# Performance work log

Measured on AMD Instinct MI355X. Metric: run time of the kernel, lower is better.

Reference implementation:

```python
import jax, jax.numpy as jnp
import numpy as np

B, S, D, H, O = 256, 64, 256, 1024, 512
N_CELLS = 3


def setup_inputs() -> dict:
    key = jax.random.key(0)
    ks = jax.random.split(key, 16)

    def u(k, shape, fan):
        return (jax.random.uniform(k, shape, jnp.float32, -1.0, 1.0) / np.float32(np.sqrt(fan)))

    inp = {"inputs": jax.random.normal(ks[0], (B, S, D), jnp.float32)}
    in_dims = [D, H, H]
    i = 1
    for c in range(N_CELLS):
        inp[f"w_ih_{c}"] = u(ks[i], (3 * H, in_dims[c]), H); i += 1
        inp[f"w_hh_{c}"] = u(ks[i], (3 * H, H), H); i += 1
        inp[f"b_ih_{c}"] = u(ks[i], (3 * H,), H); i += 1
        inp[f"b_hh_{c}"] = u(ks[i], (3 * H,), H); i += 1
    inp["lin_w"] = u(ks[13], (S, H, O), H)   # per-step linear weights (same_linear=False)
    inp["lin_b"] = u(ks[14], (S, O), H)
    return inp


def _gru_cell(x, h, w_ih, w_hh, b_ih, b_hh):
    # PyTorch GRUCell gate order: r, z, n
    gi = x @ w_ih.T + b_ih          # [B, 3H]
    gh = h @ w_hh.T + b_hh          # [B, 3H]
    i_r, i_z, i_n = jnp.split(gi, 3, axis=-1)
    h_r, h_z, h_n = jnp.split(gh, 3, axis=-1)
    r = jax.nn.sigmoid(i_r + h_r)
    z = jax.nn.sigmoid(i_z + h_z)
    n = jnp.tanh(i_n + r * h_n)
    return (1.0 - z) * n + z * h


def reference(inputs, w_ih_0, w_hh_0, b_ih_0, b_hh_0,
              w_ih_1, w_hh_1, b_ih_1, b_hh_1,
              w_ih_2, w_hh_2, b_ih_2, b_hh_2,
              lin_w, lin_b):
    params = [(w_ih_0, w_hh_0, b_ih_0, b_hh_0),
              (w_ih_1, w_hh_1, b_ih_1, b_hh_1),
              (w_ih_2, w_hh_2, b_ih_2, b_hh_2)]
    batch = inputs.shape[0]
    hdim = w_hh_0.shape[1]

    def step(hs, xs):
        x_t, wL, bL = xs              # [B,D], [H,O], [O]
        new_hs = []
        cur = x_t
        for i, (wi, wh, bi, bh) in enumerate(params):
            h = _gru_cell(cur, hs[i], wi, wh, bi, bh)
            new_hs.append(h)
            cur = h
        out = cur @ wL + bL           # [B,O]
        return tuple(new_hs), out

    h0 = tuple(jnp.zeros((batch, hdim), inputs.dtype) for _ in range(N_CELLS))
    xs = (jnp.swapaxes(inputs, 0, 1), lin_w, lin_b)  # scan over seq dim
    hs, outs = jax.lax.scan(step, h0, xs)            # outs: [S,B,O]
    return (jnp.swapaxes(outs, 0, 1), hs[0], hs[1], hs[2])
```

## Files before the change

### kernel.cpp

```cpp
#include <hip/hip_runtime.h>
#include <hip/hip_bf16.h>
#include <stdint.h>

#define B_ 256
#define S_ 64
#define D_ 256
#define H_ 1024
#define O_ 512
#define G_ 3072
#define BH_ (B_ * H_)

typedef unsigned short u16;
typedef __attribute__((ext_vector_type(8))) short bf16x8;
typedef __attribute__((ext_vector_type(4))) float f32x4;

#define MFMA16(a, b, c) __builtin_amdgcn_mfma_f32_16x16x32_bf16((a), (b), (c), 0, 0, 0)

__device__ __forceinline__ u16 f2b(float f) {
    union { float f; uint32_t u; } v; v.f = f;
    uint32_t u = v.u;
    return (u16)((u + 0x7fffu + ((u >> 16) & 1u)) >> 16);
}

__device__ __forceinline__ void gl_lds16(const u16* g, u16* l) {
    __builtin_amdgcn_global_load_lds(
        (const __attribute__((address_space(1))) unsigned int*)g,
        (__attribute__((address_space(3))) unsigned int*)l, 16, 0, 0);
}
__device__ __forceinline__ unsigned long long sysld64(const u16* p) {
    return __hip_atomic_load((const unsigned long long*)p, __ATOMIC_RELAXED, __HIP_MEMORY_SCOPE_SYSTEM);
}
__device__ __forceinline__ void sysst64(u16* p, unsigned long long v) {
    __hip_atomic_store((unsigned long long*)p, v, __ATOMIC_RELAXED, __HIP_MEMORY_SCOPE_SYSTEM);
}
__device__ __forceinline__ void waitflag(int* f, int n) {
    while (__hip_atomic_load(f, __ATOMIC_RELAXED, __HIP_MEMORY_SCOPE_SYSTEM) < n)
        __builtin_amdgcn_s_sleep(8);
    asm volatile("" ::: "memory");
}
__device__ __forceinline__ void postflag(int* f) {
    __hip_atomic_fetch_add(f, 1, __ATOMIC_RELAXED, __HIP_MEMORY_SCOPE_SYSTEM);
}


__global__ void k_conv(const float* __restrict__ s, u16* __restrict__ d, int n4) {
    int i = blockIdx.x * blockDim.x + threadIdx.x;
    int st = gridDim.x * blockDim.x;
    for (; i < n4; i += st) {
        float4 v = ((const float4*)s)[i];
        ushort4 o;
        o.x = f2b(v.x); o.y = f2b(v.y); o.z = f2b(v.z); o.w = f2b(v.w);
        ((ushort4*)d)[i] = o;
    }
}

__global__ __launch_bounds__(256) void k_twl(const float* __restrict__ w, u16* __restrict__ o) {
    __shared__ float tile[32][33];
    int bid = blockIdx.x;
    int t = bid >> 9;
    int rem = bid & 511;
    int j0 = (rem >> 4) << 5;
    int o0 = (rem & 15) << 5;
    int tx = threadIdx.x & 31, ty = threadIdx.x >> 5;
    const float* base = w + (size_t)t * (H_ * O_);
#pragma unroll
    for (int i = 0; i < 4; ++i) {
        int r = ty + (i << 3);
        tile[r][tx] = base[(size_t)(j0 + r) * O_ + o0 + tx];
    }
    __syncthreads();
    u16* ob = o + (size_t)t * (O_ * H_);
#pragma unroll
    for (int i = 0; i < 4; ++i) {
        int r = ty + (i << 3);
        ob[(size_t)(o0 + r) * H_ + j0 + tx] = f2b(tile[tx][r]);
    }
}


struct GruArgs {
    const u16* Xb;
    const u16 *Wi0, *Wh0, *Wi1, *Wh1, *Wi2, *Wh2;
    const float *bi0, *bh0, *bi1, *bh1, *bi2, *bh2;
    u16 *h0, *h1, *h2a;
    const u16* WLt;
    const float* lb;
    float* out;
    int* ready;
    int* consumed;
};

__global__ __launch_bounds__(512, 1) void k_gru(GruArgs p) {
    __shared__ u16 Wb[2][3][128 * 64];
    __shared__ u16 Ab[2][32 * 64];
    __shared__ float carry[32 * 132];

    const int w = blockIdx.x;
    const int g = w & 7;
    const int slot = w >> 3;
    const int role = slot >> 3;
    const int sub = slot & 7;
    const int b0 = g * 32;

    const int tid = threadIdx.x;
    const int wid = tid >> 6, lane = tid & 63;
    const int fr = lane & 15, kc = lane >> 4;

    const int arow = tid >> 4;
    const int acol = (tid & 15) << 2;
    const int adst = arow * 64 + ((((tid & 15) >> 1) ^ (arow & 7)) << 3) + ((tid & 1) << 2);

    int sw0 = ((kc ^ (fr & 7)) << 3);
    int sw1 = (((4 + kc) ^ (fr & 7)) << 3);

    int* ready = p.ready + g * 3 * 64;
    int* consumed = p.consumed + g * 2 * 64;

    for (int i = tid; i < 32 * 132; i += 512) carry[i] = 0.f;
    __syncthreads();

    if (role < 3) {
        const u16 *Wi, *Wh; const float *bi, *bh; int K0;
        if (role == 0)      { Wi = p.Wi0; Wh = p.Wh0; bi = p.bi0; bh = p.bh0; K0 = D_; }
        else if (role == 1) { Wi = p.Wi1; Wh = p.Wh1; bi = p.bi1; bh = p.bh1; K0 = H_; }
        else                { Wi = p.Wi2; Wh = p.Wh2; bi = p.bi2; bh = p.bh2; K0 = H_; }
        const int nXc = K0 >> 6;
        const int nC = nXc + 16;
        const int j0 = sub * 128;
        const int jme = j0 + (wid << 4) + fr;
        const float b_r = bi[jme] + bh[jme];
        const float b_z = bi[H_ + jme] + bh[H_ + jme];
        const float b_i = bi[2 * H_ + jme];
        const float b_h = bh[2 * H_ + jme];

        const u16 *A0 = nullptr, *Ah = nullptr; int ld0 = H_;
        u16* hout = nullptr;

        auto LA = [&](int c) -> unsigned long long {
            const u16* s = (c < nXc) ? (A0 + (size_t)arow * ld0 + (c << 6) + acol)
                                     : (Ah + (size_t)arow * H_ + ((c - nXc) << 6) + acol);
            return sysld64(s);
        };
        auto SW = [&](int c, int nb) {
            if (c < nXc) {
                int ko = c << 6;
#pragma unroll
                for (int hh = 0; hh < 2; ++hh) {
                    int ci = (hh << 9) + tid, jr = ci >> 3, c8 = ci & 7;
                    size_t ro = (size_t)(j0 + jr) * K0 + ko + ((c8 ^ (jr & 7)) << 3);
                    gl_lds16(Wi + ro,                     &Wb[nb][0][ci << 3]);
                    gl_lds16(Wi + (size_t)H_ * K0 + ro,   &Wb[nb][1][ci << 3]);
                    gl_lds16(Wi + (size_t)2 * H_ * K0 + ro, &Wb[nb][2][ci << 3]);
                }
            } else {
                int ko = (c - nXc) << 6;
#pragma unroll
                for (int hh = 0; hh < 2; ++hh) {
                    int ci = (hh << 9) + tid, jr = ci >> 3, c8 = ci & 7;
                    size_t ro = (size_t)(j0 + jr) * H_ + ko + ((c8 ^ (jr & 7)) << 3);
                    gl_lds16(Wh + ro,                     &Wb[nb][0][ci << 3]);
                    gl_lds16(Wh + (size_t)H_ * H_ + ro,   &Wb[nb][1][ci << 3]);
                    gl_lds16(Wh + (size_t)2 * H_ * H_ + ro, &Wb[nb][2][ci << 3]);
                }
            }
        };

        for (int t = 0; t < S_; ++t) {
            if (role == 0) {
                if (t) waitflag(&ready[0 * 64 + t - 1], 8);
                A0 = p.Xb + (size_t)b0 * (S_ * D_) + t * D_; ld0 = S_ * D_;
                Ah = p.h0 + (size_t)((t + 7) & 7) * BH_ + (size_t)b0 * H_;
                hout = p.h0 + (size_t)(t & 7) * BH_;
            } else if (role == 1) {
                waitflag(&ready[0 * 64 + t], 8);
                if (t) waitflag(&ready[1 * 64 + t - 1], 8);
                A0 = p.h0 + (size_t)(t & 7) * BH_ + (size_t)b0 * H_; ld0 = H_;
                Ah = p.h1 + (size_t)((t + 7) & 7) * BH_ + (size_t)b0 * H_;
                hout = p.h1 + (size_t)(t & 7) * BH_;
            } else {
                waitflag(&ready[1 * 64 + t], 8);
                if (t) waitflag(&ready[2 * 64 + t - 1], 8);
                A0 = p.h1 + (size_t)(t & 7) * BH_ + (size_t)b0 * H_; ld0 = H_;
                Ah = p.h2a + (size_t)t * BH_ + (size_t)b0 * H_;
                hout = p.h2a + (size_t)(t + 1) * BH_;
            }

            f32x4 accR[2] = {}, accZ[2] = {}, accI[2] = {}, accN[2] = {};

            unsigned long long la0 = LA(0), la1 = LA(1);
            *(unsigned long long*)&Ab[0][adst] = la0;
            SW(0, 0);
            la0 = LA(2);

            auto BODY = [&](int s, unsigned long long& laReg) {
                if (s + 2 < nC) asm volatile("s_waitcnt vmcnt(1)" ::: "memory");
                else            asm volatile("s_waitcnt vmcnt(0)" ::: "memory");
                asm volatile("s_waitcnt lgkmcnt(0)" ::: "memory");
                __builtin_amdgcn_s_barrier();
                __builtin_amdgcn_sched_barrier(0);
                if (s + 1 < nC) {
                    *(unsigned long long*)&Ab[(s + 1) & 1][adst] = laReg;
                    SW(s + 1, (s + 1) & 1);
                }
                if (s + 3 < nC) laReg = LA(s + 3);
                const int cur = s & 1;
                const int bo = ((wid << 4) + fr) * 64;
                bf16x8 a00 = *(const bf16x8*)&Ab[cur][fr * 64 + sw0];
                bf16x8 a01 = *(const bf16x8*)&Ab[cur][fr * 64 + sw1];
                bf16x8 a10 = *(const bf16x8*)&Ab[cur][(16 + fr) * 64 + sw0];
                bf16x8 a11 = *(const bf16x8*)&Ab[cur][(16 + fr) * 64 + sw1];
                bf16x8 r0 = *(const bf16x8*)&Wb[cur][0][bo + sw0];
                bf16x8 r1 = *(const bf16x8*)&Wb[cur][0][bo + sw1];
                bf16x8 z0 = *(const bf16x8*)&Wb[cur][1][bo + sw0];
                bf16x8 z1 = *(const bf16x8*)&Wb[cur][1][bo + sw1];
                bf16x8 q0 = *(const bf16x8*)&Wb[cur][2][bo + sw0];
                bf16x8 q1 = *(const bf16x8*)&Wb[cur][2][bo + sw1];
                __builtin_amdgcn_s_setprio(1);
                accR[0] = MFMA16(a00, r0, accR[0]); accR[0] = MFMA16(a01, r1, accR[0]);
                accR[1] = MFMA16(a10, r0, accR[1]); accR[1] = MFMA16(a11, r1, accR[1]);
                accZ[0] = MFMA16(a00, z0, accZ[0]); accZ[0] = MFMA16(a01, z1, accZ[0]);
                accZ[1] = MFMA16(a10, z0, accZ[1]); accZ[1] = MFMA16(a11, z1, accZ[1]);
                if (s < nXc) {
                    accI[0] = MFMA16(a00, q0, accI[0]); accI[0] = MFMA16(a01, q1, accI[0]);
                    accI[1] = MFMA16(a10, q0, accI[1]); accI[1] = MFMA16(a11, q1, accI[1]);
                } else {
                    accN[0] = MFMA16(a00, q0, accN[0]); accN[0] = MFMA16(a01, q1, accN[0]);
                    accN[1] = MFMA16(a10, q0, accN[1]); accN[1] = MFMA16(a11, q1, accN[1]);
                }
                __builtin_amdgcn_s_setprio(0);
            };
            for (int s = 0; s < nC; s += 2) { BODY(s, la1); BODY(s + 1, la0); }

            if (role <= 1 && t >= 8) waitflag(&consumed[role * 64 + (t - 8)], 16);

            u16* hrep = &Wb[0][0][0];
#pragma unroll
            for (int m = 0; m < 2; ++m)
#pragma unroll
                for (int i = 0; i < 4; ++i) {
                    int row = m * 16 + kc * 4 + i;
                    float rv = 1.f / (1.f + __expf(-(accR[m][i] + b_r)));
                    float zv = 1.f / (1.f + __expf(-(accZ[m][i] + b_z)));
                    float nv = tanhf(accI[m][i] + b_i + rv * (accN[m][i] + b_h));
                    float hp = carry[row * 132 + (wid << 4) + fr];
                    float hn = (1.f - zv) * nv + zv * hp;
                    carry[row * 132 + (wid << 4) + fr] = hn;
                    hrep[row * 128 + (wid << 4) + fr] = f2b(hn);
                }
            __syncthreads();
            {
                int rr = tid >> 4, jo = (tid & 15) << 3;
                unsigned long long v0 = *(const unsigned long long*)&hrep[rr * 128 + jo];
                unsigned long long v1 = *(const unsigned long long*)&hrep[rr * 128 + jo + 4];
                u16* dst = hout + (size_t)(b0 + rr) * H_ + j0 + jo;
                sysst64(dst, v0);
                sysst64(dst + 4, v1);
            }
            if (t == S_ - 1) {
                int rr = tid >> 4, jo = (tid & 15) << 3;
                float* od = p.out + (size_t)B_ * S_ * O_ + (size_t)role * BH_ +
                            (size_t)(b0 + rr) * H_ + j0 + jo;
                *(float4*)od       = *(const float4*)&carry[rr * 132 + jo];
                *(float4*)(od + 4) = *(const float4*)&carry[rr * 132 + jo + 4];
            }
            asm volatile("s_waitcnt vmcnt(0)" ::: "memory");
            __syncthreads();
            if (tid == 0) {
                postflag(&ready[role * 64 + t]);
                if (role >= 1) postflag(&consumed[(role - 1) * 64 + t]);
                if (role <= 1 && t) postflag(&consumed[role * 64 + (t - 1)]);
            }
            __syncthreads();
        }
    } else {
        const int o0 = sub << 6;
        const int nC = 16;
        const int mg = wid >> 2, og = wid & 3;
        const u16 *A0 = nullptr, *Wl = nullptr;

        auto LAl = [&](int c) -> unsigned long long {
            return sysld64(A0 + (size_t)arow * H_ + (c << 6) + acol);
        };
        auto SWl = [&](int c, int nb) {
            int orow = tid >> 3, c8 = tid & 7;
            gl_lds16(Wl + (size_t)(o0 + orow) * H_ + (c << 6) + ((c8 ^ (orow & 7)) << 3),
                     &Wb[nb][0][tid << 3]);
        };

        for (int t = 0; t < S_; ++t) {
            waitflag(&ready[2 * 64 + t], 8);
            A0 = p.h2a + (size_t)(t + 1) * BH_ + (size_t)b0 * H_;
            Wl = p.WLt + (size_t)t * (O_ * H_);

            f32x4 acc = {0.f, 0.f, 0.f, 0.f};
            unsigned long long la0 = LAl(0), la1 = LAl(1);
            *(unsigned long long*)&Ab[0][adst] = la0;
            SWl(0, 0);
            la0 = LAl(2);

            auto BODYL = [&](int s, unsigned long long& laReg) {
                if (s + 2 < nC) asm volatile("s_waitcnt vmcnt(1)" ::: "memory");
                else            asm volatile("s_waitcnt vmcnt(0)" ::: "memory");
                asm volatile("s_waitcnt lgkmcnt(0)" ::: "memory");
                __builtin_amdgcn_s_barrier();
                __builtin_amdgcn_sched_barrier(0);
                if (s + 1 < nC) {
                    *(unsigned long long*)&Ab[(s + 1) & 1][adst] = laReg;
                    SWl(s + 1, (s + 1) & 1);
                }
                if (s + 3 < nC) laReg = LAl(s + 3);
                const int cur = s & 1;
                bf16x8 a0 = *(const bf16x8*)&Ab[cur][(mg * 16 + fr) * 64 + sw0];
                bf16x8 a1 = *(const bf16x8*)&Ab[cur][(mg * 16 + fr) * 64 + sw1];
                bf16x8 w0 = *(const bf16x8*)&Wb[cur][0][(og * 16 + fr) * 64 + sw0];
                bf16x8 w1 = *(const bf16x8*)&Wb[cur][0][(og * 16 + fr) * 64 + sw1];
                __builtin_amdgcn_s_setprio(1);
                acc = MFMA16(a0, w0, acc);
                acc = MFMA16(a1, w1, acc);
                __builtin_amdgcn_s_setprio(0);
            };
            for (int s = 0; s < nC; s += 2) { BODYL(s, la1); BODYL(s + 1, la0); }

            float bb = p.lb[t * O_ + o0 + og * 16 + fr];
#pragma unroll
            for (int i = 0; i < 4; ++i) {
                int row = mg * 16 + kc * 4 + i;
                p.out[((size_t)(b0 + row) * S_ + t) * O_ + o0 + og * 16 + fr] = acc[i] + bb;
            }
        }
    }
}


extern "C" void kernel_launch(void* const* d_in, const int* in_sizes, int n_in,
                              void* d_out, int out_size, void* d_ws, size_t ws_size,
                              hipStream_t stream) {
    (void)in_sizes; (void)n_in; (void)out_size; (void)ws_size;
    const float* x   = (const float*)d_in[0];
    const float* wi0 = (const float*)d_in[1];
    const float* wh0 = (const float*)d_in[2];
    const float* bi0 = (const float*)d_in[3];
    const float* bh0 = (const float*)d_in[4];
    const float* wi1 = (const float*)d_in[5];
    const float* wh1 = (const float*)d_in[6];
    const float* bi1 = (const float*)d_in[7];
    const float* bh1 = (const float*)d_in[8];
    const float* wi2 = (const float*)d_in[9];
    const float* wh2 = (const float*)d_in[10];
    const float* bi2 = (const float*)d_in[11];
    const float* bh2 = (const float*)d_in[12];
    const float* lw  = (const float*)d_in[13];
    const float* lb  = (const float*)d_in[14];

    char* base = (char*)d_ws;
    size_t off = 0;
    auto alloc = [&](size_t bytes) {
        char* p = base + off;
        off = (off + bytes + 255) & ~(size_t)255;
        return p;
    };
    u16* Xb  = (u16*)alloc((size_t)B_ * S_ * D_ * 2);
    u16* Wi0 = (u16*)alloc((size_t)G_ * D_ * 2);
    u16* Wh0 = (u16*)alloc((size_t)G_ * H_ * 2);
    u16* Wi1 = (u16*)alloc((size_t)G_ * H_ * 2);
    u16* Wh1 = (u16*)alloc((size_t)G_ * H_ * 2);
    u16* Wi2 = (u16*)alloc((size_t)G_ * H_ * 2);
    u16* Wh2 = (u16*)alloc((size_t)G_ * H_ * 2);
    u16* h0  = (u16*)alloc((size_t)8 * BH_ * 2);
    u16* h1  = (u16*)alloc((size_t)8 * BH_ * 2);
    u16* h2a = (u16*)alloc((size_t)(S_ + 1) * BH_ * 2);
    u16* WLt = (u16*)alloc((size_t)S_ * O_ * H_ * 2);
    int* flags = (int*)alloc((size_t)(8 * 3 * 64 + 8 * 2 * 64) * 4);
    int* ready = flags;
    int* consumed = flags + 8 * 3 * 64;

    k_conv<<<1024, 256, 0, stream>>>(x,   Xb,  (B_ * S_ * D_) / 4);
    k_conv<<<1024, 256, 0, stream>>>(wi0, Wi0, (G_ * D_) / 4);
    k_conv<<<1024, 256, 0, stream>>>(wh0, Wh0, (G_ * H_) / 4);
    k_conv<<<1024, 256, 0, stream>>>(wi1, Wi1, (G_ * H_) / 4);
    k_conv<<<1024, 256, 0, stream>>>(wh1, Wh1, (G_ * H_) / 4);
    k_conv<<<1024, 256, 0, stream>>>(wi2, Wi2, (G_ * H_) / 4);
    k_conv<<<1024, 256, 0, stream>>>(wh2, Wh2, (G_ * H_) / 4);
    k_twl<<<S_ * 512, 256, 0, stream>>>(lw, WLt);
    hipMemsetAsync(h0 + (size_t)7 * BH_, 0, (size_t)BH_ * 2, stream);
    hipMemsetAsync(h1 + (size_t)7 * BH_, 0, (size_t)BH_ * 2, stream);
    hipMemsetAsync(h2a, 0, (size_t)BH_ * 2, stream);
    hipMemsetAsync(flags, 0, (size_t)(8 * 3 * 64 + 8 * 2 * 64) * 4, stream);

    GruArgs ga;
    ga.Xb = Xb;
    ga.Wi0 = Wi0; ga.Wh0 = Wh0; ga.Wi1 = Wi1; ga.Wh1 = Wh1; ga.Wi2 = Wi2; ga.Wh2 = Wh2;
    ga.bi0 = bi0; ga.bh0 = bh0; ga.bi1 = bi1; ga.bh1 = bh1; ga.bi2 = bi2; ga.bh2 = bh2;
    ga.h0 = h0; ga.h1 = h1; ga.h2a = h2a;
    ga.WLt = WLt; ga.lb = lb; ga.out = (float*)d_out;
    ga.ready = ready; ga.consumed = consumed;

    void* args[] = {&ga};
    hipLaunchCooperativeKernel((void*)k_gru, dim3(256), dim3(512), args, 0, stream);
}
```

Before: 2.919 ms.

## Remap GRU blocks so each XCD owns a hidden-column slice across all batches

Swaps the block-to-work mapping so that blocks on the same XCD (w&7) share the same weight columns (j0 = xcd*128) and iterate over batch groups. Each XCD's L2 then holds only its own slice of the weights rather than all of them. In exchange, synchronisation becomes global: ready and consumed flags wait on 64 or 128 blocks instead of 8 or 16, so each barrier now spans all XCDs. The h0/h1 ring buffers grow from 8 to 32 slots to loosen coupling between layers.

```diff
diff --git a/kernel.cpp b/kernel.cpp
--- a/kernel.cpp
+++ b/kernel.cpp
@@ -9,6 +9,7 @@
 #define O_ 512
 #define G_ 3072
 #define BH_ (B_ * H_)
+#define RING_ 32
 
 typedef unsigned short u16;
 typedef __attribute__((ext_vector_type(8))) short bf16x8;
@@ -96,11 +97,11 @@
     __shared__ float carry[32 * 132];
 
     const int w = blockIdx.x;
-    const int g = w & 7;
+    const int xcd = w & 7;
     const int slot = w >> 3;
     const int role = slot >> 3;
     const int sub = slot & 7;
-    const int b0 = g * 32;
+    const int b0 = sub * 32;
 
     const int tid = threadIdx.x;
     const int wid = tid >> 6, lane = tid & 63;
@@ -113,8 +114,8 @@
     int sw0 = ((kc ^ (fr & 7)) << 3);
     int sw1 = (((4 + kc) ^ (fr & 7)) << 3);
 
-    int* ready = p.ready + g * 3 * 64;
-    int* consumed = p.consumed + g * 2 * 64;
+    int* ready = p.ready;
+    int* consumed = p.consumed;
 
     for (int i = tid; i < 32 * 132; i += 512) carry[i] = 0.f;
     __syncthreads();
@@ -126,7 +127,7 @@
         else                { Wi = p.Wi2; Wh = p.Wh2; bi = p.bi2; bh = p.bh2; K0 = H_; }
         const int nXc = K0 >> 6;
         const int nC = nXc + 16;
-        const int j0 = sub * 128;
+        const int j0 = xcd * 128;
         const int jme = j0 + (wid << 4) + fr;
         const float b_r = bi[jme] + bh[jme];
         const float b_z = bi[H_ + jme] + bh[H_ + jme];
@@ -148,8 +149,8 @@
                 for (int hh = 0; hh < 2; ++hh) {
                     int ci = (hh << 9) + tid, jr = ci >> 3, c8 = ci & 7;
                     size_t ro = (size_t)(j0 + jr) * K0 + ko + ((c8 ^ (jr & 7)) << 3);
-                    gl_lds16(Wi + ro,                     &Wb[nb][0][ci << 3]);
-                    gl_lds16(Wi + (size_t)H_ * K0 + ro,   &Wb[nb][1][ci << 3]);
+                    gl_lds16(Wi + ro,                       &Wb[nb][0][ci << 3]);
+                    gl_lds16(Wi + (size_t)H_ * K0 + ro,     &Wb[nb][1][ci << 3]);
                     gl_lds16(Wi + (size_t)2 * H_ * K0 + ro, &Wb[nb][2][ci << 3]);
                 }
             } else {
@@ -158,8 +159,8 @@
                 for (int hh = 0; hh < 2; ++hh) {
                     int ci = (hh << 9) + tid, jr = ci >> 3, c8 = ci & 7;
                     size_t ro = (size_t)(j0 + jr) * H_ + ko + ((c8 ^ (jr & 7)) << 3);
-                    gl_lds16(Wh + ro,                     &Wb[nb][0][ci << 3]);
-                    gl_lds16(Wh + (size_t)H_ * H_ + ro,   &Wb[nb][1][ci << 3]);
+                    gl_lds16(Wh + ro,                       &Wb[nb][0][ci << 3]);
+                    gl_lds16(Wh + (size_t)H_ * H_ + ro,     &Wb[nb][1][ci << 3]);
                     gl_lds16(Wh + (size_t)2 * H_ * H_ + ro, &Wb[nb][2][ci << 3]);
                 }
             }
@@ -167,20 +168,20 @@
 
         for (int t = 0; t < S_; ++t) {
             if (role == 0) {
-                if (t) waitflag(&ready[0 * 64 + t - 1], 8);
+                if (t) waitflag(&ready[0 * 64 + t - 1], 64);
                 A0 = p.Xb + (size_t)b0 * (S_ * D_) + t * D_; ld0 = S_ * D_;
-                Ah = p.h0 + (size_t)((t + 7) & 7) * BH_ + (size_t)b0 * H_;
-                hout = p.h0 + (size_t)(t & 7) * BH_;
+                Ah = p.h0 + (size_t)((t + RING_ - 1) & (RING_ - 1)) * BH_ + (size_t)b0 * H_;
+                hout = p.h0 + (size_t)(t & (RING_ - 1)) * BH_;
             } else if (role == 1) {
-                waitflag(&ready[0 * 64 + t], 8);
-                if (t) waitflag(&ready[1 * 64 + t - 1], 8);
-                A0 = p.h0 + (size_t)(t & 7) * BH_ + (size_t)b0 * H_; ld0 = H_;
-                Ah = p.h1 + (size_t)((t + 7) & 7) * BH_ + (size_t)b0 * H_;
-                hout = p.h1 + (size_t)(t & 7) * BH_;
+                waitflag(&ready[0 * 64 + t], 64);
+                if (t) waitflag(&ready[1 * 64 + t - 1], 64);
+                A0 = p.h0 + (size_t)(t & (RING_ - 1)) * BH_ + (size_t)b0 * H_; ld0 = H_;
+                Ah = p.h1 + (size_t)((t + RING_ - 1) & (RING_ - 1)) * BH_ + (size_t)b0 * H_;
+                hout = p.h1 + (size_t)(t & (RING_ - 1)) * BH_;
             } else {
-                waitflag(&ready[1 * 64 + t], 8);
-                if (t) waitflag(&ready[2 * 64 + t - 1], 8);
-                A0 = p.h1 + (size_t)(t & 7) * BH_ + (size_t)b0 * H_; ld0 = H_;
+                waitflag(&ready[1 * 64 + t], 64);
+                if (t) waitflag(&ready[2 * 64 + t - 1], 64);
+                A0 = p.h1 + (size_t)(t & (RING_ - 1)) * BH_ + (size_t)b0 * H_; ld0 = H_;
                 Ah = p.h2a + (size_t)t * BH_ + (size_t)b0 * H_;
                 hout = p.h2a + (size_t)(t + 1) * BH_;
             }
@@ -231,7 +232,7 @@
             };
             for (int s = 0; s < nC; s += 2) { BODY(s, la1); BODY(s + 1, la0); }
 
-            if (role <= 1 && t >= 8) waitflag(&consumed[role * 64 + (t - 8)], 16);
+            if (role <= 1 && t >= RING_) waitflag(&consumed[role * 64 + (t - RING_)], 128);
 
             u16* hrep = &Wb[0][0][0];
 #pragma unroll
@@ -267,13 +268,18 @@
             __syncthreads();
             if (tid == 0) {
                 postflag(&ready[role * 64 + t]);
-                if (role >= 1) postflag(&consumed[(role - 1) * 64 + t]);
-                if (role <= 1 && t) postflag(&consumed[role * 64 + (t - 1)]);
+                if (role == 0) { if (t) postflag(&consumed[0 * 64 + t - 1]); }
+                else if (role == 1) {
+                    postflag(&consumed[0 * 64 + t]);
+                    if (t) postflag(&consumed[1 * 64 + t - 1]);
+                } else {
+                    postflag(&consumed[1 * 64 + t]);
+                }
             }
             __syncthreads();
         }
     } else {
-        const int o0 = sub << 6;
+        const int o0 = xcd << 6;
         const int nC = 16;
         const int mg = wid >> 2, og = wid & 3;
         const u16 *A0 = nullptr, *Wl = nullptr;
@@ -288,7 +294,7 @@
         };
 
         for (int t = 0; t < S_; ++t) {
-            waitflag(&ready[2 * 64 + t], 8);
+            waitflag(&ready[2 * 64 + t], 64);
             A0 = p.h2a + (size_t)(t + 1) * BH_ + (size_t)b0 * H_;
             Wl = p.WLt + (size_t)t * (O_ * H_);
 
@@ -366,13 +372,13 @@
     u16* Wh1 = (u16*)alloc((size_t)G_ * H_ * 2);
     u16* Wi2 = (u16*)alloc((size_t)G_ * H_ * 2);
     u16* Wh2 = (u16*)alloc((size_t)G_ * H_ * 2);
-    u16* h0  = (u16*)alloc((size_t)8 * BH_ * 2);
-    u16* h1  = (u16*)alloc((size_t)8 * BH_ * 2);
+    u16* h0  = (u16*)alloc((size_t)RING_ * BH_ * 2);
+    u16* h1  = (u16*)alloc((size_t)RING_ * BH_ * 2);
     u16* h2a = (u16*)alloc((size_t)(S_ + 1) * BH_ * 2);
     u16* WLt = (u16*)alloc((size_t)S_ * O_ * H_ * 2);
-    int* flags = (int*)alloc((size_t)(8 * 3 * 64 + 8 * 2 * 64) * 4);
+    int* flags = (int*)alloc((size_t)(3 * 64 + 2 * 64) * 4);
     int* ready = flags;
-    int* consumed = flags + 8 * 3 * 64;
+    int* consumed = flags + 3 * 64;
 
     k_conv<<<1024, 256, 0, stream>>>(x,   Xb,  (B_ * S_ * D_) / 4);
     k_conv<<<1024, 256, 0, stream>>>(wi0, Wi0, (G_ * D_) / 4);
@@ -382,10 +388,10 @@
     k_conv<<<1024, 256, 0, stream>>>(wi2, Wi2, (G_ * H_) / 4);
     k_conv<<<1024, 256, 0, stream>>>(wh2, Wh2, (G_ * H_) / 4);
     k_twl<<<S_ * 512, 256, 0, stream>>>(lw, WLt);
-    hipMemsetAsync(h0 + (size_t)7 * BH_, 0, (size_t)BH_ * 2, stream);
-    hipMemsetAsync(h1 + (size_t)7 * BH_, 0, (size_t)BH_ * 2, stream);
+    hipMemsetAsync(h0 + (size_t)(RING_ - 1) * BH_, 0, (size_t)BH_ * 2, stream);
+    hipMemsetAsync(h1 + (size_t)(RING_ - 1) * BH_, 0, (size_t)BH_ * 2, stream);
     hipMemsetAsync(h2a, 0, (size_t)BH_ * 2, stream);
-    hipMemsetAsync(flags, 0, (size_t)(8 * 3 * 64 + 8 * 2 * 64) * 4, stream);
+    hipMemsetAsync(flags, 0, (size_t)(3 * 64 + 2 * 64) * 4, stream);
 
     GruArgs ga;
     ga.Xb = Xb;
```

Measured after the change: 2.615 ms. 10.4% less time.
